# Kernel optimization log

Hardware: AMD Instinct MI355X
Metric: run time of the kernel (lower is better)

Reference implementation:

```python
import jax, jax.numpy as jnp
import numpy as np
from jax import lax

B, T, F = 4096, 100, 40
H_ENC, H_LAT, H_DEC = 64, 32, 64


def _lstm(x, Wih, Whh, b):
    """PyTorch-convention LSTM (gate order i,f,g,o), batch_first, zero init state.
    x: [B,T,Fin], Wih: [4H,Fin], Whh: [4H,H], b: [4H] (= b_ih + b_hh).
    Returns hidden sequence [B,T,H]."""
    H = Whh.shape[1]
    # precompute input contributions for all timesteps in one GEMM
    xg = jnp.einsum('btf,gf->btg', x, Wih) + b  # [B,T,4H]
    h0 = jnp.zeros((x.shape[0], H), dtype=x.dtype)
    c0 = jnp.zeros((x.shape[0], H), dtype=x.dtype)

    def step(carry, gx_t):
        h, c = carry
        gates = gx_t + h @ Whh.T  # [B,4H]
        i, f, g, o = jnp.split(gates, 4, axis=-1)
        c = jax.nn.sigmoid(f) * c + jax.nn.sigmoid(i) * jnp.tanh(g)
        h = jax.nn.sigmoid(o) * jnp.tanh(c)
        return (h, c), h

    _, hs = lax.scan(step, (h0, c0), jnp.swapaxes(xg, 0, 1))  # [T,B,H]
    return jnp.swapaxes(hs, 0, 1)


def setup_inputs() -> dict:
    key = jax.random.key(0)
    ks = jax.random.split(key, 8)
    s = 0.05
    return {
        'x': jax.random.normal(ks[0], (B, T, F), dtype=jnp.float32),
        'enc_Wih': jax.random.normal(ks[1], (4 * H_ENC, F), dtype=jnp.float32) * s,
        'enc_Whh': jax.random.normal(ks[2], (4 * H_ENC, H_ENC), dtype=jnp.float32) * s,
        'enc_b': jnp.zeros((4 * H_ENC,), dtype=jnp.float32),
        'lat_Wih': jax.random.normal(ks[3], (4 * H_LAT, H_ENC), dtype=jnp.float32) * s,
        'lat_Whh': jax.random.normal(ks[4], (4 * H_LAT, H_LAT), dtype=jnp.float32) * s,
        'lat_b': jnp.zeros((4 * H_LAT,), dtype=jnp.float32),
        'dec_Wih': jax.random.normal(ks[5], (4 * H_DEC, H_LAT), dtype=jnp.float32) * s,
        'dec_Whh': jax.random.normal(ks[6], (4 * H_DEC, H_DEC), dtype=jnp.float32) * s,
        'dec_b': jnp.zeros((4 * H_DEC,), dtype=jnp.float32),
        'out_W': jax.random.normal(ks[7], (F, H_DEC), dtype=jnp.float32) * s,
        'out_b': jnp.zeros((F,), dtype=jnp.float32),
    }


def reference(x, enc_Wih, enc_Whh, enc_b, lat_Wih, lat_Whh, lat_b,
              dec_Wih, dec_Whh, dec_b, out_W, out_b):
    h = _lstm(x, enc_Wih, enc_Whh, enc_b)                 # [B,T,64]
    last = h[:, -1:, :]                                   # [B,1,64]
    rep = jnp.broadcast_to(last, (h.shape[0], h.shape[1], last.shape[-1]))
    h = _lstm(rep, lat_Wih, lat_Whh, lat_b)               # [B,T,32]
    h = _lstm(h, dec_Wih, dec_Whh, dec_b)                 # [B,T,64]
    return jnp.einsum('bth,fh->btf', h, out_W) + out_b    # [B,T,40]
```

## Files before the change

kernel.cpp:

```cpp
#include <hip/hip_runtime.h>
#include <cstddef>

typedef _Float16 f16x8 __attribute__((ext_vector_type(8)));
typedef __attribute__((ext_vector_type(4))) float f32x4;

#define MFMA(a, b, c) __builtin_amdgcn_mfma_f32_16x16x32_f16((a), (b), (c), 0, 0, 0)

static constexpr float LO_SCALE = 2048.0f;
static constexpr float LO_INV   = 1.0f / 2048.0f;

static __device__ __forceinline__ unsigned f2h_bits(float f) {
  _Float16 h = (_Float16)f;
  return (unsigned)__builtin_bit_cast(unsigned short, h);
}
static __device__ __forceinline__ unsigned pack16(unsigned a, unsigned b) {
  return __builtin_amdgcn_perm(b, a, 0x05040100u);
}
static __device__ __forceinline__ void wsplit(float v, _Float16& hi, _Float16& lo) {
  _Float16 h = (_Float16)v;
  hi = h;
  lo = (_Float16)((v - (float)h) * LO_SCALE);
}
static __device__ __forceinline__ float fast_sig(float x) {
  return __builtin_amdgcn_rcpf(1.0f + __expf(-x));
}
static __device__ __forceinline__ float fast_tanh(float x) {
  return 2.0f * __builtin_amdgcn_rcpf(1.0f + __expf(-2.0f * x)) - 1.0f;
}

static __device__ __forceinline__ void lds_barrier() {
  asm volatile("s_waitcnt lgkmcnt(0)\n\ts_barrier" ::: "memory");
}

static __device__ __forceinline__ f16x8 aread(const char* base, int lane, int kc) {
  int b = lane & 15, g = lane >> 4;
  int off = (kc * 64 + g * 16) ^ ((b & 7) << 4);
  return *(const f16x8*)(base + b * 256 + off);
}
static __device__ __forceinline__ void awrite16(char* base, int b, int k, unsigned short v) {
  int off = (2 * k) ^ ((b & 7) << 4);
  *(unsigned short*)(base + b * 256 + off) = v;
}
static __device__ __forceinline__ void awrite32(char* base, int b, int k, unsigned v) {
  int off = (2 * k) ^ ((b & 7) << 4);
  *(unsigned*)(base + b * 256 + off) = v;
}

extern "C" __global__ __launch_bounds__(512, 2)
void lstm_ae_mfma9(const float* __restrict__ x,
                   const float* __restrict__ eWih, const float* __restrict__ eWhh, const float* __restrict__ eb,
                   const float* __restrict__ lWih, const float* __restrict__ lWhh, const float* __restrict__ lb,
                   const float* __restrict__ dWih, const float* __restrict__ dWhh, const float* __restrict__ db,
                   const float* __restrict__ oW,  const float* __restrict__ ob,
                   float* __restrict__ out)
{
  __shared__ __align__(16) char sA[2][4096];

  const int tid  = threadIdx.x;
  const int lane = tid & 63;
  const int w    = tid >> 6;
  const int c16  = lane & 15;
  const int p4   = lane >> 4;
  const int bbase = blockIdx.x * 16;

  {
    f32x4 z = {0.f, 0.f, 0.f, 0.f};
    *(f32x4*)(&sA[0][0] + tid * 16) = z;
  }

  f16x8 ewh[2][4], ewl[2][4];
  float ebias[2][4];
#pragma unroll
  for (int n = 0; n < 2; ++n) {
    int u = w * 8 + (c16 >> 2) * 2 + n;
    int ga = c16 & 3;
#pragma unroll
    for (int r = 0; r < 4; ++r) ebias[n][r] = eb[r * 64 + (w * 8 + p4 * 2 + n)];
#pragma unroll
    for (int kc = 0; kc < 4; ++kc) {
      f16x8 hi, lo;
#pragma unroll
      for (int e = 0; e < 8; ++e) {
        int k = kc * 32 + p4 * 8 + e;
        float v = 0.f;
        if (k < 40)       v = eWih[(ga * 64 + u) * 40 + k];
        else if (k >= 64) v = eWhh[(ga * 64 + u) * 64 + (k - 64)];
        _Float16 h, l;
        wsplit(v, h, l);
        hi[e] = h; lo[e] = l;
      }
      ewh[n][kc] = hi; ewl[n][kc] = lo;
    }
  }

  lds_barrier();

  const bool stager = (tid < 160);
  const int sb = tid / 10, sf4 = tid - (tid / 10) * 10;
  if (stager) {
    f32x4 ld = *(const f32x4*)(x + ((size_t)(bbase + sb) * 100 + 0) * 40 + sf4 * 4);
    unsigned long long pv =
        (unsigned long long)pack16(f2h_bits(ld[0]), f2h_bits(ld[1]))
      | ((unsigned long long)pack16(f2h_bits(ld[2]), f2h_bits(ld[3])) << 32);
    int off = (sf4 * 8) ^ ((sb & 7) << 4);
    *(unsigned long long*)(sA[0] + sb * 256 + off) = pv;
  }

  float cE[2] = {0.f, 0.f};
  int q = 0;
  lds_barrier();

#pragma unroll 1
  for (int t = 0; t < 100; ++t) {
    f32x4 xld;
    if (stager) {
      int tn = (t + 1 < 100) ? t + 1 : 99;
      xld = *(const f32x4*)(x + ((size_t)(bbase + sb) * 100 + tn) * 40 + sf4 * 4);
    }

    f32x4 acc[2], accL[2];
#pragma unroll
    for (int n = 0; n < 2; ++n) {
      acc[n]  = f32x4{ebias[n][0], ebias[n][1], ebias[n][2], ebias[n][3]};
      accL[n] = f32x4{0.f, 0.f, 0.f, 0.f};
    }
    const char* A = sA[q];
#pragma unroll
    for (int kc = 0; kc < 4; ++kc) {
      f16x8 a = aread(A, lane, kc);
#pragma unroll
      for (int n = 0; n < 2; ++n) {
        acc[n]  = MFMA(ewh[n][kc], a, acc[n]);
        accL[n] = MFMA(ewl[n][kc], a, accL[n]);
      }
    }

    char* AN = sA[q ^ 1];
    unsigned hb[2];
#pragma unroll
    for (int n = 0; n < 2; ++n) {
      f32x4 gv = acc[n] + accL[n] * LO_INV;
      float ii = fast_sig(gv[0]), ff = fast_sig(gv[1]);
      float gg = fast_tanh(gv[2]), oo = fast_sig(gv[3]);
      cE[n] = ff * cE[n] + ii * gg;
      float hv = oo * fast_tanh(cE[n]);
      hb[n] = f2h_bits(hv);
    }
    awrite32(AN, c16, 64 + w * 8 + p4 * 2, pack16(hb[0], hb[1]));

    if (stager) {
      unsigned long long pv =
          (unsigned long long)pack16(f2h_bits(xld[0]), f2h_bits(xld[1]))
        | ((unsigned long long)pack16(f2h_bits(xld[2]), f2h_bits(xld[3])) << 32);
      int off = (sf4 * 8) ^ ((sb & 7) << 4);
      *(unsigned long long*)(AN + sb * 256 + off) = pv;
    }
    lds_barrier();
    q ^= 1;
  }

  f32x4 xga;
  {
    int u = w * 4 + (c16 >> 2), ga = c16 & 3;
    int ul = w * 4 + p4;
    xga = f32x4{lb[ul], lb[32 + ul], lb[64 + ul], lb[96 + ul]};
    f32x4 xgaL = {0.f, 0.f, 0.f, 0.f};
#pragma unroll
    for (int kci = 0; kci < 2; ++kci) {
      f16x8 hi, lo;
#pragma unroll
      for (int e = 0; e < 8; ++e) {
        float v = lWih[(ga * 32 + u) * 64 + kci * 32 + p4 * 8 + e];
        _Float16 h, l;
        wsplit(v, h, l);
        hi[e] = h; lo[e] = l;
      }
      f16x8 a = aread(sA[q], lane, 2 + kci);
      xga  = MFMA(hi, a, xga);
      xgaL = MFMA(lo, a, xgaL);
    }
    xga = xga + xgaL * LO_INV;
  }
  lds_barrier();

  {
    f32x4 z = {0.f, 0.f, 0.f, 0.f};
    *(f32x4*)(&sA[0][0] + tid * 16) = z;
  }

  f16x8 lwh, lwl;
  {
    int u = w * 4 + (c16 >> 2), ga = c16 & 3;
    f16x8 hi, lo;
#pragma unroll
    for (int e = 0; e < 8; ++e) {
      float v = lWhh[(ga * 32 + u) * 32 + p4 * 8 + e];
      _Float16 h, l;
      wsplit(v, h, l);
      hi[e] = h; lo[e] = l;
    }
    lwh = hi; lwl = lo;
  }
  f16x8 dwh[2][3], dwl[2][3];
  float dbias[2][4];
#pragma unroll
  for (int n = 0; n < 2; ++n) {
    int u = w * 8 + (c16 >> 2) * 2 + n;
    int ga = c16 & 3;
#pragma unroll
    for (int r = 0; r < 4; ++r) dbias[n][r] = db[r * 64 + (w * 8 + p4 * 2 + n)];
#pragma unroll
    for (int kc = 0; kc < 3; ++kc) {
      f16x8 hi, lo;
#pragma unroll
      for (int e = 0; e < 8; ++e) {
        int k = kc * 32 + p4 * 8 + e;
        float v = (k < 32) ? dWih[(ga * 64 + u) * 32 + k]
                           : dWhh[(ga * 64 + u) * 64 + (k - 32)];
        _Float16 h, l;
        wsplit(v, h, l);
        hi[e] = h; lo[e] = l;
      }
      dwh[n][kc] = hi; dwl[n][kc] = lo;
    }
  }
  f16x8 pwh[2], pwl[2];
  float pbias[4];
#pragma unroll
  for (int r = 0; r < 4; ++r) {
    int f = w * 16 + p4 * 4 + r;
    pbias[r] = (w < 3 && f < 40) ? ob[f] : 0.0f;
  }
  if (w < 3) {
    int f = w * 16 + c16;
#pragma unroll
    for (int kci = 0; kci < 2; ++kci) {
      f16x8 hi, lo;
#pragma unroll
      for (int e = 0; e < 8; ++e) {
        float v = (f < 40) ? oW[f * 64 + kci * 32 + p4 * 8 + e] : 0.0f;
        _Float16 h, l;
        wsplit(v, h, l);
        hi[e] = h; lo[e] = l;
      }
      pwh[kci] = hi; pwl[kci] = lo;
    }
  }

  float cL = 0.f;
  float cD[2] = {0.f, 0.f};
  lds_barrier();

#pragma unroll 1
  for (int i = 0; i < 102; ++i) {
    const int pa = i & 1;
    f16x8 c0 = aread(sA[pa ^ 1], lane, 0);
    f16x8 d1 = aread(sA[pa], lane, 1);
    f16x8 d2 = aread(sA[pa], lane, 2);

    if (i < 100) {
      f32x4 lac = xga, lacL = {0.f, 0.f, 0.f, 0.f};
      lac  = MFMA(lwh, c0, lac);
      lacL = MFMA(lwl, c0, lacL);
      f32x4 gv = lac + lacL * LO_INV;
      float ii = fast_sig(gv[0]), ff = fast_sig(gv[1]);
      float gg = fast_tanh(gv[2]), oo = fast_sig(gv[3]);
      cL = ff * cL + ii * gg;
      float hv = oo * fast_tanh(cL);
      awrite16(sA[pa], c16, w * 4 + p4, (unsigned short)f2h_bits(hv));
    }

    if (i >= 1 && i < 101) {
      unsigned hb[2];
#pragma unroll
      for (int n = 0; n < 2; ++n) {
        f32x4 dac = f32x4{dbias[n][0], dbias[n][1], dbias[n][2], dbias[n][3]};
        f32x4 dacL = {0.f, 0.f, 0.f, 0.f};
        dac  = MFMA(dwh[n][0], c0, dac);
        dacL = MFMA(dwl[n][0], c0, dacL);
        dac  = MFMA(dwh[n][1], d1, dac);
        dacL = MFMA(dwl[n][1], d1, dacL);
        dac  = MFMA(dwh[n][2], d2, dac);
        dacL = MFMA(dwl[n][2], d2, dacL);
        f32x4 gv = dac + dacL * LO_INV;
        float ii = fast_sig(gv[0]), ff = fast_sig(gv[1]);
        float gg = fast_tanh(gv[2]), oo = fast_sig(gv[3]);
        cD[n] = ff * cD[n] + ii * gg;
        float hv = oo * fast_tanh(cD[n]);
        hb[n] = f2h_bits(hv);
      }
      awrite32(sA[pa ^ 1], c16, 32 + w * 8 + p4 * 2, pack16(hb[0], hb[1]));
    }

    if (i >= 2 && w < 3) {
      f32x4 pac = f32x4{pbias[0], pbias[1], pbias[2], pbias[3]};
      f32x4 pacL = {0.f, 0.f, 0.f, 0.f};
      pac  = MFMA(pwh[0], d1, pac);
      pacL = MFMA(pwl[0], d1, pacL);
      pac  = MFMA(pwh[1], d2, pac);
      pacL = MFMA(pwl[1], d2, pacL);
      f32x4 pv = pac + pacL * LO_INV;
#pragma unroll
      for (int r = 0; r < 4; ++r) {
        int f = w * 16 + p4 * 4 + r;
        if (f < 40)
          out[((size_t)(bbase + c16) * 100 + (i - 2)) * 40 + f] = pv[r];
      }
    }
    lds_barrier();
  }
}

extern "C" void kernel_launch(void* const* d_in, const int* in_sizes, int n_in,
                              void* d_out, int out_size, void* d_ws, size_t ws_size,
                              hipStream_t stream) {
  const float* x    = (const float*)d_in[0];
  const float* eWih = (const float*)d_in[1];
  const float* eWhh = (const float*)d_in[2];
  const float* eb   = (const float*)d_in[3];
  const float* lWih = (const float*)d_in[4];
  const float* lWhh = (const float*)d_in[5];
  const float* lb   = (const float*)d_in[6];
  const float* dWih = (const float*)d_in[7];
  const float* dWhh = (const float*)d_in[8];
  const float* db   = (const float*)d_in[9];
  const float* oW   = (const float*)d_in[10];
  const float* ob   = (const float*)d_in[11];
  float* out = (float*)d_out;

  lstm_ae_mfma9<<<256, 512, 0, stream>>>(x, eWih, eWhh, eb, lWih, lWhh, lb,
                                         dWih, dWhh, db, oW, ob, out);
}
```

Baseline: 159.0 us.

## Double threads per block to one hidden unit per wave and fuse gate math

Blocks grow from 512 to 1024 threads (16 waves), so each wave now owns 4 hidden units instead of 8. That halves the MFMA and gate work per wave on the serial recurrent critical path. The latent LSTM runs on waves 0-7 and the output projection moves to waves 13-15. The sigmoid and tanh cell math is merged into one update that shares reciprocals, cutting the number of rcp ops. In exchange, occupancy drops to one block per CU, and barriers now synchronise twice as many waves.

```diff
diff --git a/kernel.cpp b/kernel.cpp
--- a/kernel.cpp
+++ b/kernel.cpp
@@ -21,11 +21,17 @@
   hi = h;
   lo = (_Float16)((v - (float)h) * LO_SCALE);
 }
-static __device__ __forceinline__ float fast_sig(float x) {
-  return __builtin_amdgcn_rcpf(1.0f + __expf(-x));
-}
-static __device__ __forceinline__ float fast_tanh(float x) {
-  return 2.0f * __builtin_amdgcn_rcpf(1.0f + __expf(-2.0f * x)) - 1.0f;
+
+static __device__ __forceinline__ float cell_update(float gi, float gf, float gg,
+                                                    float go, float& c) {
+  float ei = __expf(-gi), ef = __expf(-gf);
+  float eg = __expf(-2.0f * gg), eo = __expf(-go);
+  float Di = 1.0f + ei, Df = 1.0f + ef, Dg = 1.0f + eg;
+  float t1  = Di * Dg;
+  float num = fmaf(1.0f - eg, Df, c * t1);
+  c = num * __builtin_amdgcn_rcpf(Df * t1);
+  float ec = __expf(-2.0f * c);
+  return (1.0f - ec) * __builtin_amdgcn_rcpf((1.0f + eo) * (1.0f + ec));
 }
 
 static __device__ __forceinline__ void lds_barrier() {
@@ -41,18 +47,14 @@
   int off = (2 * k) ^ ((b & 7) << 4);
   *(unsigned short*)(base + b * 256 + off) = v;
 }
-static __device__ __forceinline__ void awrite32(char* base, int b, int k, unsigned v) {
-  int off = (2 * k) ^ ((b & 7) << 4);
-  *(unsigned*)(base + b * 256 + off) = v;
-}
-
-extern "C" __global__ __launch_bounds__(512, 2)
-void lstm_ae_mfma9(const float* __restrict__ x,
-                   const float* __restrict__ eWih, const float* __restrict__ eWhh, const float* __restrict__ eb,
-                   const float* __restrict__ lWih, const float* __restrict__ lWhh, const float* __restrict__ lb,
-                   const float* __restrict__ dWih, const float* __restrict__ dWhh, const float* __restrict__ db,
-                   const float* __restrict__ oW,  const float* __restrict__ ob,
-                   float* __restrict__ out)
+
+extern "C" __global__ __launch_bounds__(1024, 1)
+void lstm_ae_mfma10(const float* __restrict__ x,
+                    const float* __restrict__ eWih, const float* __restrict__ eWhh, const float* __restrict__ eb,
+                    const float* __restrict__ lWih, const float* __restrict__ lWhh, const float* __restrict__ lb,
+                    const float* __restrict__ dWih, const float* __restrict__ dWhh, const float* __restrict__ db,
+                    const float* __restrict__ oW,  const float* __restrict__ ob,
+                    float* __restrict__ out)
 {
   __shared__ __align__(16) char sA[2][4096];
 
@@ -62,20 +64,19 @@
   const int c16  = lane & 15;
   const int p4   = lane >> 4;
   const int bbase = blockIdx.x * 16;
-
-  {
+  const int ga   = c16 & 3;
+
+  if (tid < 512) {
     f32x4 z = {0.f, 0.f, 0.f, 0.f};
     *(f32x4*)(&sA[0][0] + tid * 16) = z;
   }
 
-  f16x8 ewh[2][4], ewl[2][4];
-  float ebias[2][4];
-#pragma unroll
-  for (int n = 0; n < 2; ++n) {
-    int u = w * 8 + (c16 >> 2) * 2 + n;
-    int ga = c16 & 3;
-#pragma unroll
-    for (int r = 0; r < 4; ++r) ebias[n][r] = eb[r * 64 + (w * 8 + p4 * 2 + n)];
+  f16x8 ewh[4], ewl[4];
+  float ebias[4];
+  {
+    int u = w * 4 + (c16 >> 2);
+#pragma unroll
+    for (int r = 0; r < 4; ++r) ebias[r] = eb[r * 64 + (w * 4 + p4)];
 #pragma unroll
     for (int kc = 0; kc < 4; ++kc) {
       f16x8 hi, lo;
@@ -89,7 +90,7 @@
         wsplit(v, h, l);
         hi[e] = h; lo[e] = l;
       }
-      ewh[n][kc] = hi; ewl[n][kc] = lo;
+      ewh[kc] = hi; ewl[kc] = lo;
     }
   }
 
@@ -106,7 +107,7 @@
     *(unsigned long long*)(sA[0] + sb * 256 + off) = pv;
   }
 
-  float cE[2] = {0.f, 0.f};
+  float cE = 0.f;
   int q = 0;
   lds_barrier();
 
@@ -118,35 +119,22 @@
       xld = *(const f32x4*)(x + ((size_t)(bbase + sb) * 100 + tn) * 40 + sf4 * 4);
     }
 
-    f32x4 acc[2], accL[2];
-#pragma unroll
-    for (int n = 0; n < 2; ++n) {
-      acc[n]  = f32x4{ebias[n][0], ebias[n][1], ebias[n][2], ebias[n][3]};
-      accL[n] = f32x4{0.f, 0.f, 0.f, 0.f};
-    }
+    f32x4 acc  = f32x4{ebias[0], ebias[1], ebias[2], ebias[3]};
+    f32x4 accL = {0.f, 0.f, 0.f, 0.f};
     const char* A = sA[q];
 #pragma unroll
     for (int kc = 0; kc < 4; ++kc) {
       f16x8 a = aread(A, lane, kc);
-#pragma unroll
-      for (int n = 0; n < 2; ++n) {
-        acc[n]  = MFMA(ewh[n][kc], a, acc[n]);
-        accL[n] = MFMA(ewl[n][kc], a, accL[n]);
-      }
+      acc  = MFMA(ewh[kc], a, acc);
+      accL = MFMA(ewl[kc], a, accL);
     }
 
     char* AN = sA[q ^ 1];
-    unsigned hb[2];
-#pragma unroll
-    for (int n = 0; n < 2; ++n) {
-      f32x4 gv = acc[n] + accL[n] * LO_INV;
-      float ii = fast_sig(gv[0]), ff = fast_sig(gv[1]);
-      float gg = fast_tanh(gv[2]), oo = fast_sig(gv[3]);
-      cE[n] = ff * cE[n] + ii * gg;
-      float hv = oo * fast_tanh(cE[n]);
-      hb[n] = f2h_bits(hv);
-    }
-    awrite32(AN, c16, 64 + w * 8 + p4 * 2, pack16(hb[0], hb[1]));
+    {
+      f32x4 gv = acc + accL * LO_INV;
+      float hv = cell_update(gv[0], gv[1], gv[2], gv[3], cE);
+      awrite16(AN, c16, 64 + w * 4 + p4, (unsigned short)f2h_bits(hv));
+    }
 
     if (stager) {
       unsigned long long pv =
@@ -159,9 +147,9 @@
     q ^= 1;
   }
 
-  f32x4 xga;
-  {
-    int u = w * 4 + (c16 >> 2), ga = c16 & 3;
+  f32x4 xga = {0.f, 0.f, 0.f, 0.f};
+  if (w < 8) {
+    int u = w * 4 + (c16 >> 2);
     int ul = w * 4 + p4;
     xga = f32x4{lb[ul], lb[32 + ul], lb[64 + ul], lb[96 + ul]};
     f32x4 xgaL = {0.f, 0.f, 0.f, 0.f};
@@ -183,14 +171,14 @@
   }
   lds_barrier();
 
-  {
+  if (tid < 512) {
     f32x4 z = {0.f, 0.f, 0.f, 0.f};
     *(f32x4*)(&sA[0][0] + tid * 16) = z;
   }
 
-  f16x8 lwh, lwl;
-  {
-    int u = w * 4 + (c16 >> 2), ga = c16 & 3;
+  f16x8 lwh = {}, lwl = {};
+  if (w < 8) {
+    int u = w * 4 + (c16 >> 2);
     f16x8 hi, lo;
 #pragma unroll
     for (int e = 0; e < 8; ++e) {
@@ -201,14 +189,12 @@
     }
     lwh = hi; lwl = lo;
   }
-  f16x8 dwh[2][3], dwl[2][3];
-  float dbias[2][4];
-#pragma unroll
-  for (int n = 0; n < 2; ++n) {
-    int u = w * 8 + (c16 >> 2) * 2 + n;
-    int ga = c16 & 3;
-#pragma unroll
-    for (int r = 0; r < 4; ++r) dbias[n][r] = db[r * 64 + (w * 8 + p4 * 2 + n)];
+  f16x8 dwh[3], dwl[3];
+  float dbias[4];
+  {
+    int u = w * 4 + (c16 >> 2);
+#pragma unroll
+    for (int r = 0; r < 4; ++r) dbias[r] = db[r * 64 + (w * 4 + p4)];
 #pragma unroll
     for (int kc = 0; kc < 3; ++kc) {
       f16x8 hi, lo;
@@ -221,18 +207,19 @@
         wsplit(v, h, l);
         hi[e] = h; lo[e] = l;
       }
-      dwh[n][kc] = hi; dwl[n][kc] = lo;
-    }
-  }
-  f16x8 pwh[2], pwl[2];
+      dwh[kc] = hi; dwl[kc] = lo;
+    }
+  }
+  f16x8 pwh[2] = {}, pwl[2] = {};
   float pbias[4];
+  const int wp = w - 13;
 #pragma unroll
   for (int r = 0; r < 4; ++r) {
-    int f = w * 16 + p4 * 4 + r;
-    pbias[r] = (w < 3 && f < 40) ? ob[f] : 0.0f;
-  }
-  if (w < 3) {
-    int f = w * 16 + c16;
+    int f = wp * 16 + p4 * 4 + r;
+    pbias[r] = (w >= 13 && f < 40) ? ob[f] : 0.0f;
+  }
+  if (w >= 13) {
+    int f = wp * 16 + c16;
 #pragma unroll
     for (int kci = 0; kci < 2; ++kci) {
       f16x8 hi, lo;
@@ -247,8 +234,7 @@
     }
   }
 
-  float cL = 0.f;
-  float cD[2] = {0.f, 0.f};
+  float cL = 0.f, cD = 0.f;
   lds_barrier();
 
 #pragma unroll 1
@@ -258,41 +244,30 @@
     f16x8 d1 = aread(sA[pa], lane, 1);
     f16x8 d2 = aread(sA[pa], lane, 2);
 
-    if (i < 100) {
+    if (i < 100 && w < 8) {
       f32x4 lac = xga, lacL = {0.f, 0.f, 0.f, 0.f};
       lac  = MFMA(lwh, c0, lac);
       lacL = MFMA(lwl, c0, lacL);
       f32x4 gv = lac + lacL * LO_INV;
-      float ii = fast_sig(gv[0]), ff = fast_sig(gv[1]);
-      float gg = fast_tanh(gv[2]), oo = fast_sig(gv[3]);
-      cL = ff * cL + ii * gg;
-      float hv = oo * fast_tanh(cL);
+      float hv = cell_update(gv[0], gv[1], gv[2], gv[3], cL);
       awrite16(sA[pa], c16, w * 4 + p4, (unsigned short)f2h_bits(hv));
     }
 
     if (i >= 1 && i < 101) {
-      unsigned hb[2];
-#pragma unroll
-      for (int n = 0; n < 2; ++n) {
-        f32x4 dac = f32x4{dbias[n][0], dbias[n][1], dbias[n][2], dbias[n][3]};
-        f32x4 dacL = {0.f, 0.f, 0.f, 0.f};
-        dac  = MFMA(dwh[n][0], c0, dac);
-        dacL = MFMA(dwl[n][0], c0, dacL);
-        dac  = MFMA(dwh[n][1], d1, dac);
-        dacL = MFMA(dwl[n][1], d1, dacL);
-        dac  = MFMA(dwh[n][2], d2, dac);
-        dacL = MFMA(dwl[n][2], d2, dacL);
-        f32x4 gv = dac + dacL * LO_INV;
-        float ii = fast_sig(gv[0]), ff = fast_sig(gv[1]);
-        float gg = fast_tanh(gv[2]), oo = fast_sig(gv[3]);
-        cD[n] = ff * cD[n] + ii * gg;
-        float hv = oo * fast_tanh(cD[n]);
-        hb[n] = f2h_bits(hv);
-      }
-      awrite32(sA[pa ^ 1], c16, 32 + w * 8 + p4 * 2, pack16(hb[0], hb[1]));
-    }
-
-    if (i >= 2 && w < 3) {
+      f32x4 dac = f32x4{dbias[0], dbias[1], dbias[2], dbias[3]};
+      f32x4 dacL = {0.f, 0.f, 0.f, 0.f};
+      dac  = MFMA(dwh[0], c0, dac);
+      dacL = MFMA(dwl[0], c0, dacL);
+      dac  = MFMA(dwh[1], d1, dac);
+      dacL = MFMA(dwl[1], d1, dacL);
+      dac  = MFMA(dwh[2], d2, dac);
+      dacL = MFMA(dwl[2], d2, dacL);
+      f32x4 gv = dac + dacL * LO_INV;
+      float hv = cell_update(gv[0], gv[1], gv[2], gv[3], cD);
+      awrite16(sA[pa ^ 1], c16, 32 + w * 4 + p4, (unsigned short)f2h_bits(hv));
+    }
+
+    if (i >= 2 && w >= 13) {
       f32x4 pac = f32x4{pbias[0], pbias[1], pbias[2], pbias[3]};
       f32x4 pacL = {0.f, 0.f, 0.f, 0.f};
       pac  = MFMA(pwh[0], d1, pac);
@@ -302,7 +277,7 @@
       f32x4 pv = pac + pacL * LO_INV;
 #pragma unroll
       for (int r = 0; r < 4; ++r) {
-        int f = w * 16 + p4 * 4 + r;
+        int f = wp * 16 + p4 * 4 + r;
         if (f < 40)
           out[((size_t)(bbase + c16) * 100 + (i - 2)) * 40 + f] = pv[r];
       }
@@ -328,6 +303,6 @@
   const float* ob   = (const float*)d_in[11];
   float* out = (float*)d_out;
 
-  lstm_ae_mfma9<<<256, 512, 0, stream>>>(x, eWih, eWhh, eb, lWih, lWhh, lb,
-                                         dWih, dWhh, db, oW, ob, out);
-}
+  lstm_ae_mfma10<<<256, 1024, 0, stream>>>(x, eWih, eWhh, eb, lWih, lWhh, lb,
+                                           dWih, dWhh, db, oW, ob, out);
+}
```

After: 167.6 us. +5.4%, slower.
